# Optimization experiments

Hardware: AMD Instinct MI355X
Metric: run time of the kernel (lower is better)

Reference implementation:

```python
import jax, jax.numpy as jnp
import numpy as np

B, C, N, H = 8, 256, 1024, 8

def setup_inputs() -> dict:
    key = jax.random.key(0)
    ks = jax.random.split(key, 6)
    x = jax.random.normal(ks[0], (B, C, 3, N), jnp.float32)
    scale = 1.0 / np.sqrt(C).astype(np.float32)
    Wq = jax.random.normal(ks[1], (C, C), jnp.float32) * scale
    Wk = jax.random.normal(ks[2], (C, C), jnp.float32) * scale
    Wv = jax.random.normal(ks[3], (C, C), jnp.float32) * scale
    Wp = jax.random.normal(ks[4], (C, C), jnp.float32) * scale
    mask = jax.random.randint(ks[5], (B, N), 0, 2).astype(bool)  # True = padded
    return {"x": x, "Wq": Wq, "Wk": Wk, "Wv": Wv, "Wp": Wp, "mask": mask}

def _vn_linear(W, x):
    # VNLinear: channel-mixing linear (no bias) over the C axis of [B, C, 3, N]
    return jnp.einsum('oc,bcdn->bodn', W, x)

def _to_heads(t):
    # [B, C, 3, N] -> [B, H, N, (C//H)*3]
    hd = C // H
    return t.reshape(B, H, hd, 3, N).transpose(0, 1, 4, 2, 3).reshape(B, H, N, hd * 3)

def reference(x, Wq, Wk, Wv, Wp, mask):
    hd = C // H
    D = hd * 3
    q = _to_heads(_vn_linear(Wq, x))
    k = _to_heads(_vn_linear(Wk, x))
    v = _to_heads(_vn_linear(Wv, x))
    att = jnp.einsum('bhnd,bhmd->bhnm', q, k) * (1.0 / np.sqrt(D).astype(np.float32))
    att = jnp.where(mask[:, None, None, :], -jnp.inf, att)
    att = jax.nn.softmax(att, axis=-1)
    y = jnp.einsum('bhnm,bhmd->bhnd', att, v)
    # [B, H, N, D] -> [B, H, D, N] -> [B, H, hd, 3, N] -> [B, C, 3, N]
    y = y.transpose(0, 1, 3, 2).reshape(B, H, hd, 3, N).reshape(B, C, 3, N)
    return _vn_linear(Wp, y)
```

## Files before the change

kernel.cpp:

```cpp
#include <hip/hip_runtime.h>
#include <hip/hip_bf16.h>
#include <math.h>

#define B_ 8
#define C_ 256
#define N_ 1024
#define H_ 8
#define DH 96
#define BHN (C_*3*N_)
#define SC 0.10206207261596575f
#define SCL2 0.14722193f

typedef _Float16 half8 __attribute__((ext_vector_type(8)));
typedef float f32x4 __attribute__((ext_vector_type(4)));
typedef float f32x16 __attribute__((ext_vector_type(16)));

typedef __attribute__((address_space(1))) void gvoid;
typedef __attribute__((address_space(3))) void lvoid;
__device__ inline void gl_lds16(const _Float16* g, _Float16* l) {
  __builtin_amdgcn_global_load_lds((gvoid*)g, (lvoid*)l, 16, 0, 0);
}

__device__ inline float ex2(float x) { return __builtin_amdgcn_exp2f(x); }

typedef __fp16 fp16x2 __attribute__((ext_vector_type(2)));
union H2U { fp16x2 h2; unsigned u; };
__device__ inline unsigned pkh(float a, float b) {
  H2U x; x.h2 = __builtin_amdgcn_cvt_pkrtz(a, b); return x.u;
}
union PF { half8 v; unsigned u[4]; };

__device__ inline void plswap(unsigned& a, unsigned& b) {
  asm volatile("v_permlane32_swap_b32 %0, %1" : "+v"(a), "+v"(b));
}

__global__ void mask_bits_kernel(const unsigned* __restrict__ mraw,
                                 unsigned long long* __restrict__ mb) {
  __shared__ int notI, notF;
  if (threadIdx.x == 0) { notI = 0; notF = 0; }
  __syncthreads();
  int li = 0, lf = 0;
  for (int i = threadIdx.x; i < 2048; i += 256) {
    unsigned w = mraw[i];
    if (w > 1u) li = 1;
    if (w != 0u && w != 0x3F800000u) lf = 1;
  }
  if (li) atomicOr(&notI, 1);
  if (lf) atomicOr(&notF, 1);
  __syncthreads();
  const int tid = threadIdx.x;
  if (tid < 128) {
    int base = tid * 64;
    unsigned long long bits = 0;
    if (!notI) {
      for (int j = 0; j < 64; ++j)
        bits |= (unsigned long long)(mraw[base + j] & 1u) << j;
    } else if (!notF) {
      for (int j = 0; j < 64; ++j)
        bits |= (unsigned long long)(mraw[base + j] != 0u ? 1 : 0) << j;
    } else {
      const unsigned char* m8 = (const unsigned char*)mraw;
      for (int j = 0; j < 64; ++j)
        bits |= (unsigned long long)(m8[base + j] ? 1 : 0) << j;
    }
    mb[tid] = bits;
  }
}

__global__ void convw_kernel(const float* __restrict__ Wq,
                             const float* __restrict__ Wk,
                             const float* __restrict__ Wv,
                             const float* __restrict__ Wp,
                             _Float16* __restrict__ Wh) {
  int idx = blockIdx.x * 256 + threadIdx.x;
  int e0 = idx * 8;
  const float* src = (e0 < 65536) ? Wq
                   : (e0 < 131072) ? Wk
                   : (e0 < 196608) ? Wv : Wp;
  int off = e0 & 65535;
  float4 a = *(const float4*)&src[off];
  float4 b = *(const float4*)&src[off + 4];
  _Float16 t[8] = {(_Float16)a.x, (_Float16)a.y, (_Float16)a.z, (_Float16)a.w,
                   (_Float16)b.x, (_Float16)b.y, (_Float16)b.z, (_Float16)b.w};
  *(uint4*)&Wh[e0] = *(uint4*)t;
}

__global__ __launch_bounds__(256) void convxt_kernel(
    const float* __restrict__ x, _Float16* __restrict__ XT) {
  __shared__ _Float16 T[64][65];
  const int m0 = blockIdx.x * 64;
  const int c0 = blockIdx.y * 64;
  const int b = blockIdx.z;
  const float* xb = x + (size_t)b * BHN;
  _Float16* ob = XT + (size_t)b * BHN;
  const int t = threadIdx.x;
#pragma unroll
  for (int i = 0; i < 16; ++i) {
    int e = t + i * 256;
    int c = e >> 6, m = e & 63;
    T[m][c] = (_Float16)xb[(size_t)(c0 + c) * 3072 + m0 + m];
  }
  __syncthreads();
#pragma unroll
  for (int i = 0; i < 2; ++i) {
    int e = t + i * 256;
    int m = e >> 3, ch = e & 7;
    _Float16 tmp[8];
#pragma unroll
    for (int j = 0; j < 8; ++j) tmp[j] = T[m][ch * 8 + j];
    *(uint4*)&ob[(size_t)(m0 + m) * 256 + c0 + ch * 8] = *(uint4*)tmp;
  }
}

template <int MODE>
__global__ __launch_bounds__(256, 4) void mgemm_kernel(
    const _Float16* __restrict__ Wh, int woff,
    const _Float16* __restrict__ Xn,
    _Float16* __restrict__ O0, _Float16* __restrict__ O1,
    _Float16* __restrict__ O2, float* __restrict__ Of, int nw) {
  const int zz = blockIdx.z;
  const int w = zz % nw;
  const int b = zz / nw;
  const _Float16* Wb = Wh + (size_t)(woff + w) * 65536;
  const _Float16* Bb = Xn + (size_t)b * BHN;
  const int o0 = blockIdx.y * 128;
  const int bn0 = blockIdx.x * 128;

  __shared__ __align__(16) _Float16 Ah[4096];
  __shared__ __align__(16) _Float16 Bh[4096];

  const int tid = threadIdx.x;
  const int wave = tid >> 6;
  const int lane = tid & 63;
  const int lg = lane >> 4, ll = lane & 15;
  const int wm = wave >> 1, wn = wave & 1;
  const int r0 = tid >> 2, c4 = tid & 3;

  f32x4 acc[4][4];
#pragma unroll
  for (int mi = 0; mi < 4; ++mi)
#pragma unroll
    for (int ni = 0; ni < 4; ++ni) acc[mi][ni] = (f32x4){0.f, 0.f, 0.f, 0.f};

  for (int k0 = 0; k0 < 256; k0 += 32) {
    gl_lds16(Wb + (size_t)(o0 + r0) * 256 + k0 + c4 * 8, &Ah[wave * 512]);
    gl_lds16(Wb + (size_t)(o0 + 64 + r0) * 256 + k0 + c4 * 8,
             &Ah[2048 + wave * 512]);
    gl_lds16(Bb + (size_t)(bn0 + r0) * 256 + k0 + c4 * 8, &Bh[wave * 512]);
    gl_lds16(Bb + (size_t)(bn0 + 64 + r0) * 256 + k0 + c4 * 8,
             &Bh[2048 + wave * 512]);
    __syncthreads();
    half8 af[4], bf[4];
#pragma unroll
    for (int mi = 0; mi < 4; ++mi)
      af[mi] = *(const half8*)&Ah[(wm * 64 + mi * 16 + ll) * 32 + lg * 8];
#pragma unroll
    for (int ni = 0; ni < 4; ++ni)
      bf[ni] = *(const half8*)&Bh[(wn * 64 + ni * 16 + ll) * 32 + lg * 8];
#pragma unroll
    for (int mi = 0; mi < 4; ++mi)
#pragma unroll
      for (int ni = 0; ni < 4; ++ni)
        acc[mi][ni] = __builtin_amdgcn_mfma_f32_16x16x32_f16(
            af[mi], bf[ni], acc[mi][ni], 0, 0, 0);
    __syncthreads();
  }

#pragma unroll
  for (int mi = 0; mi < 4; ++mi) {
#pragma unroll
    for (int ni = 0; ni < 4; ++ni) {
      int o = o0 + wm * 64 + mi * 16 + lg * 4;
      int mcol = bn0 + wn * 64 + ni * 16 + ll;
      if constexpr (MODE == 1) {
        float* Ofb = Of + (size_t)b * BHN;
#pragma unroll
        for (int r = 0; r < 4; ++r)
          Ofb[(size_t)(o + r) * 3072 + mcol] = acc[mi][ni][r];
      } else {
        const int h = o >> 5, i = o & 31;
        const int dd = mcol >> 10, tok = mcol & 1023;
        const size_t bh8 = (size_t)(b * 8 + h);
        if (w == 2) {
          int tt = tok >> 6, kk = tok & 63;
          int kt = kk >> 4, hi2 = (kk >> 3) & 1, e = kk & 7;
          size_t base = ((((bh8 * 16 + tt) * 4 + kt) * 3 + dd) * 512) +
                        (size_t)i * 16 + hi2 * 8 + e;
#pragma unroll
          for (int r = 0; r < 4; ++r)
            O2[base + r * 16] = (_Float16)acc[mi][ni][r];
        } else {
          int dperm = dd * 32 + i;
          int pp = dperm >> 3, j0 = i & 7;
          int ks = pp >> 1, hif = pp & 1;
          float qs = (w == 0) ? SCL2 : 1.0f;
          _Float16 t4[4];
#pragma unroll
          for (int r = 0; r < 4; ++r) t4[r] = (_Float16)(acc[mi][ni][r] * qs);
          size_t idx;
          if (w == 0) {
            idx = ((bh8 * 32 + (tok >> 5)) * 6 + ks) * 512 +
                  (size_t)(tok & 31) * 16 + hif * 8 + j0;
            *(uint2*)&O0[idx] = *(uint2*)t4;
          } else {
            idx = ((bh8 * 16 + (tok >> 6)) * 6 + ks) * 1024 +
                  (size_t)(tok & 63) * 16 + hif * 8 + j0;
            *(uint2*)&O1[idx] = *(uint2*)t4;
          }
        }
      }
    }
  }
}

__global__ __launch_bounds__(256, 2) void attn_kernel(
    const _Float16* __restrict__ Qp, const _Float16* __restrict__ Kp,
    const _Float16* __restrict__ Vp,
    const unsigned long long* __restrict__ mbits,
    _Float16* __restrict__ yT) {
  const int gid = blockIdx.x;
  const int bh = gid & 63;
  const int qt = gid >> 6;
  const int b = bh >> 3, h = bh & 7;
  const int n0 = qt * 128;

  const int tid = threadIdx.x;
  const int lane = tid & 63;
  const int wave = tid >> 6;
  const int hi = lane >> 5;
  const int lq = lane & 31;
  const int wq0 = wave * 32;

  const size_t bh8 = (size_t)(b * 8 + h);
  const int lo16 = lq * 16 + hi * 8;

  const _Float16* Qb = Qp + (bh8 * 32 + (qt * 4 + wave)) * 6 * 512 + lo16;
  half8 qf[6];
#pragma unroll
  for (int ks = 0; ks < 6; ++ks) qf[ks] = *(const half8*)(Qb + ks * 512);

  const _Float16* Kh = Kp + bh8 * 98304 + lo16;
  const _Float16* Vh = Vp + bh8 * 98304 + lo16;

  half8 kf[6][2];
  auto loadK = [&](int t) {
    const _Float16* Kt = Kh + t * 6144;
#pragma unroll
    for (int ks = 0; ks < 6; ++ks) {
      kf[ks][0] = *(const half8*)(Kt + ks * 1024);
      kf[ks][1] = *(const half8*)(Kt + ks * 1024 + 512);
    }
  };
  loadK(0);

  float M = 0.f, Lh = 0.f;
  f32x16 yacc[3];
#pragma unroll
  for (int dt = 0; dt < 3; ++dt)
#pragma unroll
    for (int r = 0; r < 16; ++r) yacc[dt][r] = 0.f;

  for (int t = 0; t < 16; ++t) {
    const _Float16* Vt = Vh + t * 6144;
    half8 vf[4][3];
#pragma unroll
    for (int kt = 0; kt < 4; ++kt)
#pragma unroll
      for (int dt = 0; dt < 3; ++dt)
        vf[kt][dt] = *(const half8*)(Vt + (kt * 3 + dt) * 512);

    const unsigned long long m64 = mbits[b * 16 + t];

    f32x16 s[2];
#pragma unroll
    for (int r = 0; r < 16; ++r) { s[0][r] = 0.f; s[1][r] = 0.f; }
    __builtin_amdgcn_s_setprio(1);
#pragma unroll
    for (int ks = 0; ks < 6; ++ks) {
      s[0] = __builtin_amdgcn_mfma_f32_32x32x16_f16(kf[ks][0], qf[ks], s[0],
                                                    0, 0, 0);
      s[1] = __builtin_amdgcn_mfma_f32_32x32x16_f16(kf[ks][1], qf[ks], s[1],
                                                    0, 0, 0);
    }
    __builtin_amdgcn_s_setprio(0);

    if (t + 1 < 16) loadK(t + 1);

    float mx = -1e30f;
#pragma unroll
    for (int nt = 0; nt < 2; ++nt) {
      unsigned wm = (unsigned)(m64 >> (nt * 32 + 4 * hi));
#pragma unroll
      for (int r = 0; r < 16; ++r) {
        float sv = s[nt][r];
        sv = ((wm >> ((r & 3) + 8 * (r >> 2))) & 1u) ? -1e30f : sv;
        s[nt][r] = sv;
        mx = fmaxf(mx, sv);
      }
    }
    if (__any(mx > M + 12.f)) {
      float mx2 = fmaxf(mx, __shfl_xor(mx, 32));
      float newM = fmaxf(M, mx2);
      float corr = ex2(M - newM);
      M = newM;
      Lh *= corr;
#pragma unroll
      for (int dt = 0; dt < 3; ++dt)
#pragma unroll
        for (int r = 0; r < 16; ++r) yacc[dt][r] *= corr;
    }
    float psum = 0.f;
#pragma unroll
    for (int nt = 0; nt < 2; ++nt)
#pragma unroll
      for (int r = 0; r < 16; ++r) {
        float p = ex2(s[nt][r] - M);
        s[nt][r] = p;
        psum += p;
      }
    Lh += psum;

#pragma unroll
    for (int nt = 0; nt < 2; ++nt) {
#pragma unroll
      for (int hf = 0; hf < 2; ++hf) {
        const int bs = hf * 8;
        unsigned A0 = pkh(s[nt][bs + 0], s[nt][bs + 1]);
        unsigned A1 = pkh(s[nt][bs + 2], s[nt][bs + 3]);
        unsigned B0 = pkh(s[nt][bs + 4], s[nt][bs + 5]);
        unsigned B1 = pkh(s[nt][bs + 6], s[nt][bs + 7]);
        plswap(A0, B0);
        plswap(A1, B1);
        PF pf;
        pf.u[0] = A0;
        pf.u[1] = A1;
        pf.u[2] = B0;
        pf.u[3] = B1;
        const int kt = nt * 2 + hf;
        __builtin_amdgcn_s_setprio(1);
#pragma unroll
        for (int dt = 0; dt < 3; ++dt)
          yacc[dt] = __builtin_amdgcn_mfma_f32_32x32x16_f16(
              vf[kt][dt], pf.v, yacc[dt], 0, 0, 0);
        __builtin_amdgcn_s_setprio(0);
      }
    }
  }

  float L = Lh + __shfl_xor(Lh, 32);
  float inv = (L > 0.f) ? 1.f / L : 0.f;
  _Float16* yb = yT + (size_t)b * BHN;
#pragma unroll
  for (int dt = 0; dt < 3; ++dt) {
    _Float16* rowp =
        yb + (size_t)(dt * 1024 + n0 + wq0 + lq) * 256 + h * 32 + hi * 4;
#pragma unroll
    for (int g = 0; g < 4; ++g) {
      _Float16 t4[4];
#pragma unroll
      for (int j = 0; j < 4; ++j)
        t4[j] = (_Float16)(yacc[dt][g * 4 + j] * inv);
      *(uint2*)(rowp + g * 8) = *(uint2*)t4;
    }
  }
}

extern "C" void kernel_launch(void* const* d_in, const int* in_sizes, int n_in,
                              void* d_out, int out_size, void* d_ws,
                              size_t ws_size, hipStream_t stream) {
  const float* x = (const float*)d_in[0];
  const float* Wq = (const float*)d_in[1];
  const float* Wk = (const float*)d_in[2];
  const float* Wv = (const float*)d_in[3];
  const float* Wp = (const float*)d_in[4];
  const unsigned* mask = (const unsigned*)d_in[5];
  float* out = (float*)d_out;

  _Float16* Wh = (_Float16*)d_ws;
  _Float16* XT = Wh + 4 * 65536;
  _Float16* Qp = XT + (size_t)B_ * BHN;
  _Float16* Kp = Qp + (size_t)B_ * BHN;
  _Float16* Vp = Kp + (size_t)B_ * BHN;
  _Float16* yT = Vp + (size_t)B_ * BHN;
  unsigned long long* mb = (unsigned long long*)(yT + (size_t)B_ * BHN);

  mask_bits_kernel<<<1, 256, 0, stream>>>(mask, mb);
  convw_kernel<<<128, 256, 0, stream>>>(Wq, Wk, Wv, Wp, Wh);
  convxt_kernel<<<dim3(48, 4, B_), 256, 0, stream>>>(x, XT);

  dim3 g1(24, 2, B_ * 3);
  mgemm_kernel<0><<<g1, 256, 0, stream>>>(Wh, 0, XT, Qp, Kp, Vp, nullptr, 3);

  attn_kernel<<<dim3(512), 256, 0, stream>>>(Qp, Kp, Vp, mb, yT);

  dim3 g3(24, 2, B_);
  mgemm_kernel<1><<<g3, 256, 0, stream>>>(Wh, 3, yT, nullptr, nullptr, nullptr,
                                          out, 1);
}
```

Baseline: 93.83 us.

## Merge prep kernels into one launch and widen GEMM K-tile with swizzled LDS

Folds the mask-bit, weight-conversion and x-transpose kernels into a single prep launch, using an extra z-slice for the small side jobs. This removes two kernel launches and their serialization gaps. The channel-mixing GEMM now stages 64-wide K tiles instead of 32, with an XOR swizzle on LDS chunks so fragment reads avoid bank conflicts, and runs half as many barrier pairs per tile. LDS per block doubles to 32 KB, which may limit occupancy under the 4-blocks launch bound.

Measured after the change: 90.29 us. -3.8%, faster.

```diff
diff --git a/kernel.cpp b/kernel.cpp
--- a/kernel.cpp
+++ b/kernel.cpp
@@ -34,59 +34,61 @@
   asm volatile("v_permlane32_swap_b32 %0, %1" : "+v"(a), "+v"(b));
 }
 
-__global__ void mask_bits_kernel(const unsigned* __restrict__ mraw,
-                                 unsigned long long* __restrict__ mb) {
-  __shared__ int notI, notF;
-  if (threadIdx.x == 0) { notI = 0; notF = 0; }
-  __syncthreads();
-  int li = 0, lf = 0;
-  for (int i = threadIdx.x; i < 2048; i += 256) {
-    unsigned w = mraw[i];
-    if (w > 1u) li = 1;
-    if (w != 0u && w != 0x3F800000u) lf = 1;
-  }
-  if (li) atomicOr(&notI, 1);
-  if (lf) atomicOr(&notF, 1);
-  __syncthreads();
-  const int tid = threadIdx.x;
-  if (tid < 128) {
-    int base = tid * 64;
-    unsigned long long bits = 0;
-    if (!notI) {
-      for (int j = 0; j < 64; ++j)
-        bits |= (unsigned long long)(mraw[base + j] & 1u) << j;
-    } else if (!notF) {
-      for (int j = 0; j < 64; ++j)
-        bits |= (unsigned long long)(mraw[base + j] != 0u ? 1 : 0) << j;
-    } else {
-      const unsigned char* m8 = (const unsigned char*)mraw;
-      for (int j = 0; j < 64; ++j)
-        bits |= (unsigned long long)(m8[base + j] ? 1 : 0) << j;
-    }
-    mb[tid] = bits;
-  }
-}
-
-__global__ void convw_kernel(const float* __restrict__ Wq,
-                             const float* __restrict__ Wk,
-                             const float* __restrict__ Wv,
-                             const float* __restrict__ Wp,
-                             _Float16* __restrict__ Wh) {
-  int idx = blockIdx.x * 256 + threadIdx.x;
-  int e0 = idx * 8;
-  const float* src = (e0 < 65536) ? Wq
-                   : (e0 < 131072) ? Wk
-                   : (e0 < 196608) ? Wv : Wp;
-  int off = e0 & 65535;
-  float4 a = *(const float4*)&src[off];
-  float4 b = *(const float4*)&src[off + 4];
-  _Float16 t[8] = {(_Float16)a.x, (_Float16)a.y, (_Float16)a.z, (_Float16)a.w,
-                   (_Float16)b.x, (_Float16)b.y, (_Float16)b.z, (_Float16)b.w};
-  *(uint4*)&Wh[e0] = *(uint4*)t;
-}
-
-__global__ __launch_bounds__(256) void convxt_kernel(
-    const float* __restrict__ x, _Float16* __restrict__ XT) {
+__global__ __launch_bounds__(256) void prep_kernel(
+    const float* __restrict__ x, _Float16* __restrict__ XT,
+    const float* __restrict__ Wq, const float* __restrict__ Wk,
+    const float* __restrict__ Wv, const float* __restrict__ Wp,
+    _Float16* __restrict__ Wh, const unsigned* __restrict__ mraw,
+    unsigned long long* __restrict__ mb) {
+  if (blockIdx.z == 8) {
+    int bid = blockIdx.y * 48 + blockIdx.x;
+    if (bid < 128) {
+      int idx = bid * 256 + threadIdx.x;
+      int e0 = idx * 8;
+      const float* src = (e0 < 65536) ? Wq
+                       : (e0 < 131072) ? Wk
+                       : (e0 < 196608) ? Wv : Wp;
+      int off = e0 & 65535;
+      float4 a = *(const float4*)&src[off];
+      float4 b = *(const float4*)&src[off + 4];
+      _Float16 t[8] = {(_Float16)a.x, (_Float16)a.y, (_Float16)a.z,
+                       (_Float16)a.w, (_Float16)b.x, (_Float16)b.y,
+                       (_Float16)b.z, (_Float16)b.w};
+      *(uint4*)&Wh[e0] = *(uint4*)t;
+    } else if (bid == 128) {
+      __shared__ int notI, notF;
+      if (threadIdx.x == 0) { notI = 0; notF = 0; }
+      __syncthreads();
+      int li = 0, lf = 0;
+      for (int i = threadIdx.x; i < 2048; i += 256) {
+        unsigned w = mraw[i];
+        if (w > 1u) li = 1;
+        if (w != 0u && w != 0x3F800000u) lf = 1;
+      }
+      if (li) atomicOr(&notI, 1);
+      if (lf) atomicOr(&notF, 1);
+      __syncthreads();
+      const int tid = threadIdx.x;
+      if (tid < 128) {
+        int base = tid * 64;
+        unsigned long long bits = 0;
+        if (!notI) {
+          for (int j = 0; j < 64; ++j)
+            bits |= (unsigned long long)(mraw[base + j] & 1u) << j;
+        } else if (!notF) {
+          for (int j = 0; j < 64; ++j)
+            bits |= (unsigned long long)(mraw[base + j] != 0u ? 1 : 0) << j;
+        } else {
+          const unsigned char* m8 = (const unsigned char*)mraw;
+          for (int j = 0; j < 64; ++j)
+            bits |= (unsigned long long)(m8[base + j] ? 1 : 0) << j;
+        }
+        mb[tid] = bits;
+      }
+    }
+    return;
+  }
+
   __shared__ _Float16 T[64][65];
   const int m0 = blockIdx.x * 64;
   const int c0 = blockIdx.y * 64;
@@ -126,15 +128,14 @@
   const int o0 = blockIdx.y * 128;
   const int bn0 = blockIdx.x * 128;
 
-  __shared__ __align__(16) _Float16 Ah[4096];
-  __shared__ __align__(16) _Float16 Bh[4096];
+  __shared__ __align__(16) _Float16 Ah[8192];
+  __shared__ __align__(16) _Float16 Bh[8192];
 
   const int tid = threadIdx.x;
   const int wave = tid >> 6;
   const int lane = tid & 63;
   const int lg = lane >> 4, ll = lane & 15;
   const int wm = wave >> 1, wn = wave & 1;
-  const int r0 = tid >> 2, c4 = tid & 3;
 
   f32x4 acc[4][4];
 #pragma unroll
@@ -142,27 +143,40 @@
 #pragma unroll
     for (int ni = 0; ni < 4; ++ni) acc[mi][ni] = (f32x4){0.f, 0.f, 0.f, 0.f};
 
-  for (int k0 = 0; k0 < 256; k0 += 32) {
-    gl_lds16(Wb + (size_t)(o0 + r0) * 256 + k0 + c4 * 8, &Ah[wave * 512]);
-    gl_lds16(Wb + (size_t)(o0 + 64 + r0) * 256 + k0 + c4 * 8,
-             &Ah[2048 + wave * 512]);
-    gl_lds16(Bb + (size_t)(bn0 + r0) * 256 + k0 + c4 * 8, &Bh[wave * 512]);
-    gl_lds16(Bb + (size_t)(bn0 + 64 + r0) * 256 + k0 + c4 * 8,
-             &Bh[2048 + wave * 512]);
+  for (int k0 = 0; k0 < 256; k0 += 64) {
+#pragma unroll
+    for (int i = 0; i < 4; ++i) {
+      int e = tid + i * 256;
+      int r = e >> 3, cch = e & 7;
+      int srcc = cch ^ (r & 7);
+      _Float16* dst = &Ah[(size_t)(i * 256 + wave * 64) * 8];
+      gl_lds16(Wb + (size_t)(o0 + r) * 256 + k0 + srcc * 8, dst);
+      _Float16* dstb = &Bh[(size_t)(i * 256 + wave * 64) * 8];
+      gl_lds16(Bb + (size_t)(bn0 + r) * 256 + k0 + srcc * 8, dstb);
+    }
     __syncthreads();
-    half8 af[4], bf[4];
-#pragma unroll
-    for (int mi = 0; mi < 4; ++mi)
-      af[mi] = *(const half8*)&Ah[(wm * 64 + mi * 16 + ll) * 32 + lg * 8];
-#pragma unroll
-    for (int ni = 0; ni < 4; ++ni)
-      bf[ni] = *(const half8*)&Bh[(wn * 64 + ni * 16 + ll) * 32 + lg * 8];
-#pragma unroll
-    for (int mi = 0; mi < 4; ++mi)
-#pragma unroll
-      for (int ni = 0; ni < 4; ++ni)
-        acc[mi][ni] = __builtin_amdgcn_mfma_f32_16x16x32_f16(
-            af[mi], bf[ni], acc[mi][ni], 0, 0, 0);
+#pragma unroll
+    for (int kk = 0; kk < 2; ++kk) {
+      half8 af[4], bf[4];
+#pragma unroll
+      for (int mi = 0; mi < 4; ++mi) {
+        int row = wm * 64 + mi * 16 + ll;
+        int ch = (kk * 4 + lg) ^ (row & 7);
+        af[mi] = *(const half8*)&Ah[row * 64 + ch * 8];
+      }
+#pragma unroll
+      for (int ni = 0; ni < 4; ++ni) {
+        int row = wn * 64 + ni * 16 + ll;
+        int ch = (kk * 4 + lg) ^ (row & 7);
+        bf[ni] = *(const half8*)&Bh[row * 64 + ch * 8];
+      }
+#pragma unroll
+      for (int mi = 0; mi < 4; ++mi)
+#pragma unroll
+        for (int ni = 0; ni < 4; ++ni)
+          acc[mi][ni] = __builtin_amdgcn_mfma_f32_16x16x32_f16(
+              af[mi], bf[ni], acc[mi][ni], 0, 0, 0);
+    }
     __syncthreads();
   }
 
@@ -384,9 +398,8 @@
   _Float16* yT = Vp + (size_t)B_ * BHN;
   unsigned long long* mb = (unsigned long long*)(yT + (size_t)B_ * BHN);
 
-  mask_bits_kernel<<<1, 256, 0, stream>>>(mask, mb);
-  convw_kernel<<<128, 256, 0, stream>>>(Wq, Wk, Wv, Wp, Wh);
-  convxt_kernel<<<dim3(48, 4, B_), 256, 0, stream>>>(x, XT);
+  prep_kernel<<<dim3(48, 4, 9), 256, 0, stream>>>(x, XT, Wq, Wk, Wv, Wp, Wh,
+                                                  mask, mb);
 
   dim3 g1(24, 2, B_ * 3);
   mgemm_kernel<0><<<g1, 256, 0, stream>>>(Wh, 0, XT, Qp, Kp, Vp, nullptr, 3);
```
